# Performance work log

Hardware: AMD Instinct MI355X
Metric: run time of the kernel (lower is better)

The kernel has to match this reference:

```python
import jax, jax.numpy as jnp
import numpy as np

B, T, I, H, O = 64, 2048, 16, 256, 1


def _gru_layer(x, Wih, Whh, bih, bhh):
    # x: [B, T, in]; Wih: [3H, in]; Whh: [3H, H]
    xg = jnp.einsum('bti,gi->btg', x, Wih) + bih  # [B, T, 3H] precomputed input gates

    def step(h, xg_t):
        gh = h @ Whh.T + bhh  # [B, 3H]
        xr, xz, xn = jnp.split(xg_t, 3, axis=-1)
        hr, hz, hn = jnp.split(gh, 3, axis=-1)
        r = jax.nn.sigmoid(xr + hr)
        z = jax.nn.sigmoid(xz + hz)
        n = jnp.tanh(xn + r * hn)
        h_new = (1.0 - z) * n + z * h
        return h_new, h_new

    h0 = jnp.zeros((x.shape[0], Whh.shape[1]), dtype=x.dtype)
    _, hs = jax.lax.scan(step, h0, jnp.swapaxes(xg, 0, 1))  # [T, B, H]
    return jnp.swapaxes(hs, 0, 1)  # [B, T, H]


def setup_inputs() -> dict:
    key = jax.random.key(0)
    ks = jax.random.split(key, 8)

    def xavier(k, shape):
        fan_out, fan_in = shape
        lim = float(np.sqrt(6.0 / (fan_in + fan_out)))
        return jax.random.uniform(k, shape, jnp.float32, -lim, lim)

    return {
        'x': jax.random.normal(ks[0], (B, T, I), jnp.float32),
        'Wih0': xavier(ks[1], (3 * H, I)),
        'Whh0': xavier(ks[2], (3 * H, H)),
        'bih0': jnp.zeros((3 * H,), jnp.float32),
        'bhh0': jnp.zeros((3 * H,), jnp.float32),
        'Wih1': xavier(ks[3], (3 * H, H)),
        'Whh1': xavier(ks[4], (3 * H, H)),
        'bih1': jnp.zeros((3 * H,), jnp.float32),
        'bhh1': jnp.zeros((3 * H,), jnp.float32),
        'W1': xavier(ks[5], (H, H)),
        'b1': jnp.zeros((H,), jnp.float32),
        'W2': xavier(ks[6], (O, H)),
        'b2': jnp.zeros((O,), jnp.float32),
    }


def reference(x, Wih0, Whh0, bih0, bhh0, Wih1, Whh1, bih1, bhh1, W1, b1, W2, b2):
    h1 = _gru_layer(x, Wih0, Whh0, bih0, bhh0)    # layer 0: [B, T, H]
    h2 = _gru_layer(h1, Wih1, Whh1, bih1, bhh1)   # layer 1: [B, T, H]
    r = jax.nn.relu(jnp.einsum('bth,oh->bto', h2, W1) + b1)
    out = jnp.einsum('bth,oh->bto', r, W2) + b2
    return jax.nn.relu(out)  # final relu in forward, [B, T, O]
```

## Files before the change

### kernel.cpp

```cpp
#include <hip/hip_runtime.h>
#include <hip/hip_fp16.h>
#include <stdint.h>

#define B_ 64
#define T_ 2048
#define I_ 16
#define H_ 256
#define G_ 768

#define REC_SMEM 156736

typedef _Float16 f16;
typedef _Float16 half2_t __attribute__((ext_vector_type(2)));
typedef uint32_t u32x4 __attribute__((ext_vector_type(4)));
typedef uint32_t u32x2 __attribute__((ext_vector_type(2)));

__device__ __forceinline__ float fast_rcp(float x) {
#if __has_builtin(__builtin_amdgcn_rcpf)
    return __builtin_amdgcn_rcpf(x);
#else
    return 1.0f / x;
#endif
}
__device__ __forceinline__ float sigmoid_f(float x) {
    return fast_rcp(1.0f + __expf(-x));
}
__device__ __forceinline__ float tanh_f(float x) {
    float e = __expf(2.0f * x);
    return 1.0f - 2.0f * fast_rcp(e + 1.0f);
}

__device__ __forceinline__ float fdot2(uint32_t a, uint32_t b, float c) {
#if __has_builtin(__builtin_amdgcn_fdot2)
    return __builtin_amdgcn_fdot2(__builtin_bit_cast(half2_t, a),
                                  __builtin_bit_cast(half2_t, b), c, false);
#else
    half2_t ha = __builtin_bit_cast(half2_t, a), hb = __builtin_bit_cast(half2_t, b);
    return c + (float)ha.x * (float)hb.x + (float)ha.y * (float)hb.y;
#endif
}
__device__ __forceinline__ float dot_u4(u32x4 w, u32x4 h, float acc) {
    acc = fdot2(w.x, h.x, acc);
    acc = fdot2(w.y, h.y, acc);
    acc = fdot2(w.z, h.z, acc);
    acc = fdot2(w.w, h.w, acc);
    return acc;
}

__global__ __launch_bounds__(256) void cvt_weights(const float* __restrict__ whh0,
                                                   const float* __restrict__ whh1,
                                                   const float* __restrict__ wih1,
                                                   const float* __restrict__ w1,
                                                   uint32_t* __restrict__ out) {
    int idx = blockIdx.x * 256 + threadIdx.x;
    if (idx >= 294912) return;
    if (idx < 163840) {
        const float* w = (idx < 81920) ? whh0 : whh1;
        int l = (idx < 81920) ? idx : idx - 81920;
        if (l < 65536) {
            int u4 = l >> 2, d = l & 3;
            int P = u4 >> 9, t = u4 & 511;
            int j = t >> 1, hf = t & 1;
            int row = (P < 16) ? (256 + j) : (512 + j);
            int u = (P < 16) ? P : P - 16;
            const float* s = w + (size_t)row * 256 + hf * 128 + u * 8 + d * 2;
            half2_t h;
            h.x = (f16)s[0];
            h.y = (f16)s[1];
            out[idx] = __builtin_bit_cast(uint32_t, h);
        } else {
            int l2 = l - 65536;
            int P8 = l2 >> 10, wd = l2 & 1023;
            int t = wd >> 1, piece = wd & 1;
            int j = t >> 1, hf = t & 1;
            const float* s = w + (size_t)j * 256 + hf * 128 + P8 * 8 + piece * 4;
            uint32_t dw = 0;
            #pragma unroll
            for (int k = 0; k < 4; ++k) {
                f16 hh = (f16)s[k];
                uint16_t hb = __builtin_bit_cast(uint16_t, hh);
                uint16_t r8 = (uint16_t)((hb + 0x7F + ((hb >> 8) & 1)) >> 8);
                dw |= (uint32_t)(r8 & 0xFF) << (8 * k);
            }
            out[idx] = dw;
        }
    } else if (idx < 262144) {
        int local = idx - 163840;
        int u4 = local >> 2, d = local & 3;
        int k8 = u4 / 768, g = u4 - k8 * 768;
        const float* s = wih1 + (size_t)g * 256 + k8 * 8 + d * 2;
        half2_t h; h.x = (f16)s[0]; h.y = (f16)s[1];
        out[idx] = __builtin_bit_cast(uint32_t, h);
    } else {
        int local = idx - 262144;
        int u4 = local >> 2, d = local & 3;
        int k8 = u4 >> 8, g = u4 & 255;
        const float* s = w1 + (size_t)g * 256 + k8 * 8 + d * 2;
        half2_t h; h.x = (f16)s[0]; h.y = (f16)s[1];
        out[idx] = __builtin_bit_cast(uint32_t, h);
    }
}


__device__ __forceinline__ void xg0_body(const float* __restrict__ x,
        const float* __restrict__ wih0, const float* __restrict__ bih0,
        float* __restrict__ xg, int t0, int C, int blk, char* smem) {
    float (*xs)[16] = (float(*)[16])smem;
    int tid = threadIdx.x;
    int m0 = blk * 64;
    if (tid < 256) {
        int r = tid >> 2, c4 = (tid & 3) * 4;
        int m = m0 + r;
        int b = m / C, tl = m - b * C;
        float4 v = *(const float4*)(x + (size_t)(b * T_ + t0 + tl) * I_ + c4);
        *(float4*)&xs[r][c4] = v;
    }
    __syncthreads();
    for (int g = tid; g < G_; g += 512) {
        const float4* wr = (const float4*)(wih0 + (size_t)g * I_);
        float4 w0 = wr[0], w1 = wr[1], w2 = wr[2], w3 = wr[3];
        float bias = bih0[g];
        float* outp = xg + (size_t)m0 * G_ + g;
        for (int m = 0; m < 64; ++m) {
            const float4* xr4 = (const float4*)xs[m];
            float4 a0 = xr4[0], a1 = xr4[1], a2 = xr4[2], a3 = xr4[3];
            float acc = bias;
            acc += a0.x*w0.x + a0.y*w0.y + a0.z*w0.z + a0.w*w0.w;
            acc += a1.x*w1.x + a1.y*w1.y + a1.z*w1.z + a1.w*w1.w;
            acc += a2.x*w2.x + a2.y*w2.y + a2.z*w2.z + a2.w*w2.w;
            acc += a3.x*w3.x + a3.y*w3.y + a3.z*w3.z + a3.w*w3.w;
            outp[(size_t)m * G_] = acc;
        }
    }
}

__device__ __forceinline__ void xg1_body(const f16* __restrict__ h1,
        const uint32_t* __restrict__ wih1T, const float* __restrict__ bih1,
        float* __restrict__ xg, int C, int lgC, int blk, char* smem) {
    u32x4 (*hs)[32] = (u32x4(*)[32])smem;
    int tid = threadIdx.x;
    int m0 = (blk & (C - 1)) * 64;
    int gbase = (blk >> lgC) * 256;
    const u32x4* hsrc = (const u32x4*)h1 + (size_t)m0 * 32;
    #pragma unroll
    for (int it = 0; it < 4; ++it) {
        int o = tid + it * 512;
        hs[o >> 5][o & 31] = hsrc[o];
    }
    __syncthreads();
    int gg = tid & 31, mg = tid >> 5;
    const u32x4* wt = (const u32x4*)wih1T;
    float acc[8][4];
    #pragma unroll
    for (int i = 0; i < 8; ++i)
        #pragma unroll
        for (int r = 0; r < 4; ++r) acc[i][r] = 0.0f;
    for (int k8 = 0; k8 < 32; ++k8) {
        u32x4 w[8], h[4];
        #pragma unroll
        for (int i = 0; i < 8; ++i) w[i] = wt[(size_t)k8 * 768 + gbase + gg + 32 * i];
        #pragma unroll
        for (int r = 0; r < 4; ++r) h[r] = hs[mg * 4 + r][k8];
        #pragma unroll
        for (int i = 0; i < 8; ++i)
            #pragma unroll
            for (int r = 0; r < 4; ++r)
                acc[i][r] = dot_u4(w[i], h[r], acc[i][r]);
    }
    #pragma unroll
    for (int i = 0; i < 8; ++i) {
        int g = gbase + gg + 32 * i;
        float bias = bih1[g];
        #pragma unroll
        for (int r = 0; r < 4; ++r)
            xg[(size_t)(m0 + mg * 4 + r) * G_ + g] = acc[i][r] + bias;
    }
}

__device__ __forceinline__ void reg_body(const f16* __restrict__ h2,
        const uint32_t* __restrict__ w1T, const float* __restrict__ b1,
        const float* __restrict__ w2, const float* __restrict__ b2,
        float* __restrict__ out, int t0, int C, int lgC, int blk, char* smem) {
    u32x4 (*hs)[32] = (u32x4(*)[32])smem;
    float (*red)[4] = (float(*)[4])(smem + 32768);
    int tid = threadIdx.x;
    int m0 = blk * 64;
    const u32x4* hsrc = (const u32x4*)h2 + (size_t)m0 * 32;
    #pragma unroll
    for (int it = 0; it < 4; ++it) {
        int o = tid + it * 512;
        hs[o >> 5][o & 31] = hsrc[o];
    }
    __syncthreads();
    int gg = tid & 31, mg = tid >> 5;
    const u32x4* wt = (const u32x4*)w1T;
    float acc[8][4];
    #pragma unroll
    for (int i = 0; i < 8; ++i)
        #pragma unroll
        for (int r = 0; r < 4; ++r) acc[i][r] = 0.0f;
    for (int k8 = 0; k8 < 32; ++k8) {
        u32x4 w[8], h[4];
        #pragma unroll
        for (int i = 0; i < 8; ++i) w[i] = wt[(size_t)k8 * 256 + gg + 32 * i];
        #pragma unroll
        for (int r = 0; r < 4; ++r) h[r] = hs[mg * 4 + r][k8];
        #pragma unroll
        for (int i = 0; i < 8; ++i)
            #pragma unroll
            for (int r = 0; r < 4; ++r)
                acc[i][r] = dot_u4(w[i], h[r], acc[i][r]);
    }
    float pv[4] = {0, 0, 0, 0};
    #pragma unroll
    for (int i = 0; i < 8; ++i) {
        int g = gg + 32 * i;
        float bias = b1[g], w2g = w2[g];
        #pragma unroll
        for (int r = 0; r < 4; ++r)
            pv[r] += w2g * fmaxf(acc[i][r] + bias, 0.0f);
    }
    #pragma unroll
    for (int r = 0; r < 4; ++r) {
        pv[r] += __shfl_xor(pv[r], 1, 64);
        pv[r] += __shfl_xor(pv[r], 2, 64);
        pv[r] += __shfl_xor(pv[r], 4, 64);
        pv[r] += __shfl_xor(pv[r], 8, 64);
        pv[r] += __shfl_xor(pv[r], 16, 64);
    }
    if (gg == 0) {
        #pragma unroll
        for (int r = 0; r < 4; ++r) red[mg][r] = pv[r];
    }
    __syncthreads();
    if (tid < 64) {
        int m = m0 + tid;
        float v = fmaxf(red[tid >> 2][tid & 3] + b2[0], 0.0f);
        int b = m >> lgC, tl = m & (C - 1);
        out[(size_t)b * T_ + t0 + tl] = v;
    }
}

__device__ __forceinline__ void rec_body(const uint32_t* __restrict__ whh,
        const float* __restrict__ bhh, const float* __restrict__ xg,
        f16* __restrict__ hout, float* __restrict__ state,
        int b, int C, char* smem) {
    int tid = threadIdx.x;
    int j = tid >> 1, hf = tid & 1;
    const u32x4* wb = (const u32x4*)whh;
    const u32x2* w8 = (const u32x2*)(whh + 65536);
    u32x4* wlds = (u32x4*)smem;
    u32x4 (*hq)[2][17] = (u32x4(*)[2][17])(smem + 155648);

    #pragma unroll
    for (int s = 0; s < 16; ++s)
        wlds[s * 512 + tid] = wb[(16 + s) * 512 + tid];
    #pragma unroll
    for (int s = 0; s < 3; ++s)
        wlds[(16 + s) * 512 + tid] = wb[(12 + s) * 512 + tid];

    u32x4 Z0  = wb[ 0 * 512 + tid], Z1  = wb[ 1 * 512 + tid];
    u32x4 Z2  = wb[ 2 * 512 + tid], Z3  = wb[ 3 * 512 + tid];
    u32x4 Z4  = wb[ 4 * 512 + tid], Z5  = wb[ 5 * 512 + tid];
    u32x4 Z6  = wb[ 6 * 512 + tid], Z7  = wb[ 7 * 512 + tid];
    u32x4 Z8  = wb[ 8 * 512 + tid], Z9  = wb[ 9 * 512 + tid];
    u32x4 Z10 = wb[10 * 512 + tid], Z11 = wb[11 * 512 + tid];

    float h_old = 0.0f, bhr = 0.0f, bhz = 0.0f, bhn = 0.0f;
    if (hf == 0) {
        h_old = state[b * 256 + j];
        bhr = bhh[j]; bhz = bhh[256 + j]; bhn = bhh[512 + j];
        ((f16*)&hq[0][j >> 7][0])[j & 127] = (f16)h_old;
    }
    __syncthreads();

    const float* xgt = xg + (size_t)b * C * G_;
    f16* hob = hout + (size_t)b * C * H_;
    const u32x4* nl = wlds + tid;

    for (int tl = 0; tl < C; ++tl) {
        int p = tl & 1;
        u32x2 F0  = w8[ 0 * 512 + tid], F1  = w8[ 1 * 512 + tid];
        u32x2 F2  = w8[ 2 * 512 + tid], F3  = w8[ 3 * 512 + tid];
        u32x2 F4  = w8[ 4 * 512 + tid], F5  = w8[ 5 * 512 + tid];
        u32x2 F6  = w8[ 6 * 512 + tid], F7  = w8[ 7 * 512 + tid];
        u32x2 F8  = w8[ 8 * 512 + tid], F9  = w8[ 9 * 512 + tid];
        u32x2 F10 = w8[10 * 512 + tid], F11 = w8[11 * 512 + tid];
        u32x2 F12 = w8[12 * 512 + tid], F13 = w8[13 * 512 + tid];
        u32x2 F14 = w8[14 * 512 + tid], F15 = w8[15 * 512 + tid];
        u32x4 SZ = wb[15 * 512 + tid];
        float xr = 0, xz = 0, xn = 0;
        if (hf == 0) { xr = xgt[j]; xz = xgt[256 + j]; xn = xgt[512 + j]; }

        const u32x4* hp = &hq[p][hf][0];
        float aR = 0.0f, aZ = 0.0f, aN = 0.0f;

#define PU(u, ZS) { u32x4 hv = hp[u]; \
        aN = dot_u4(nl[(u) * 512], hv, aN); \
        aZ = dot_u4(ZS, hv, aZ); \
        u32x4 wr; \
        wr.x = __byte_perm(F##u.x, 0u, 0x1404); \
        wr.y = __byte_perm(F##u.x, 0u, 0x3424); \
        wr.z = __byte_perm(F##u.y, 0u, 0x1404); \
        wr.w = __byte_perm(F##u.y, 0u, 0x3424); \
        aR = dot_u4(wr, hv, aR); }

        PU(0,  Z0)  PU(1,  Z1)  PU(2,  Z2)  PU(3,  Z3)
        PU(4,  Z4)  PU(5,  Z5)  PU(6,  Z6)  PU(7,  Z7)
        PU(8,  Z8)  PU(9,  Z9)  PU(10, Z10) PU(11, Z11)
        PU(12, nl[16 * 512]) PU(13, nl[17 * 512]) PU(14, nl[18 * 512])
        PU(15, SZ)
#undef PU

        aR += __shfl_xor(aR, 1, 64);
        aZ += __shfl_xor(aZ, 1, 64);
        aN += __shfl_xor(aN, 1, 64);

        if (hf == 0) {
            float r = sigmoid_f(xr + aR + bhr);
            float z = sigmoid_f(xz + aZ + bhz);
            float n = tanh_f(xn + r * (aN + bhn));
            h_old = z * (h_old - n) + n;
            f16 hh = (f16)h_old;
            hob[(size_t)tl * H_ + j] = hh;
            ((f16*)&hq[p ^ 1][j >> 7][0])[j & 127] = hh;
        }
        __syncthreads();
        xgt += G_;
    }
    if (hf == 0) state[b * 256 + j] = h_old;
}

__global__ __launch_bounds__(512)
__attribute__((amdgpu_waves_per_eu(2, 2)))
void fused_step(int i, int nC, int C, int lgC,
        const float* __restrict__ x,
        const float* __restrict__ wih0, const float* __restrict__ bih0,
        const uint32_t* __restrict__ whh0, const float* __restrict__ bhh0,
        const uint32_t* __restrict__ whh1, const float* __restrict__ bhh1,
        const uint32_t* __restrict__ wih1T, const float* __restrict__ bih1,
        const uint32_t* __restrict__ w1T, const float* __restrict__ b1,
        const float* __restrict__ w2, const float* __restrict__ b2,
        float* __restrict__ xg0a, float* __restrict__ xg0b,
        float* __restrict__ xg1a, float* __restrict__ xg1b,
        f16* __restrict__ h1a, f16* __restrict__ h1b,
        f16* __restrict__ h2a, f16* __restrict__ h2b,
        float* __restrict__ st0, float* __restrict__ st1,
        float* __restrict__ out) {
    extern __shared__ __align__(16) char smem[];
    int blk = blockIdx.x;
    if (blk < 64) {
        if (i >= nC) return;
        rec_body(whh0, bhh0, (i & 1) ? xg0b : xg0a,
                 (i & 1) ? h1b : h1a, st0, blk, C, smem);
    } else if (blk < 128) {
        int c = i - 2;
        if (c < 0 || c >= nC) return;
        rec_body(whh1, bhh1, (c & 1) ? xg1b : xg1a,
                 (c & 1) ? h2b : h2a, st1, blk - 64, C, smem);
    } else if (blk < 128 + C) {
        int c = i + 1;
        if (c >= nC) return;
        xg0_body(x, wih0, bih0, (c & 1) ? xg0b : xg0a, c * C, C, blk - 128, smem);
    } else if (blk < 128 + 4 * C) {
        int c = i - 1;
        if (c < 0 || c >= nC) return;
        xg1_body((c & 1) ? h1b : h1a, wih1T, bih1,
                 (c & 1) ? xg1b : xg1a, C, lgC, blk - 128 - C, smem);
    } else {
        int c = i - 3;
        if (c < 0 || c >= nC) return;
        reg_body((c & 1) ? h2b : h2a, w1T, b1, w2, b2, out, c * C, C, lgC,
                 blk - 128 - 4 * C, smem);
    }
}

__global__ __launch_bounds__(512) void xg0_stand(const float* __restrict__ x,
        const float* __restrict__ wih0, const float* __restrict__ bih0,
        float* __restrict__ xg, int t0, int C) {
    __shared__ __align__(16) char smem[4096];
    xg0_body(x, wih0, bih0, xg, t0, C, blockIdx.x, smem);
}

extern "C" void kernel_launch(void* const* d_in, const int* in_sizes, int n_in,
                              void* d_out, int out_size, void* d_ws, size_t ws_size,
                              hipStream_t stream) {
    const float* x    = (const float*)d_in[0];
    const float* Wih0 = (const float*)d_in[1];
    const float* Whh0 = (const float*)d_in[2];
    const float* bih0 = (const float*)d_in[3];
    const float* bhh0 = (const float*)d_in[4];
    const float* Wih1 = (const float*)d_in[5];
    const float* Whh1 = (const float*)d_in[6];
    const float* bih1 = (const float*)d_in[7];
    const float* bhh1 = (const float*)d_in[8];
    const float* W1   = (const float*)d_in[9];
    const float* b1   = (const float*)d_in[10];
    const float* W2   = (const float*)d_in[11];
    const float* b2   = (const float*)d_in[12];
    float* out = (float*)d_out;

    hipFuncSetAttribute(reinterpret_cast<const void*>(fused_step),
                        hipFuncAttributeMaxDynamicSharedMemorySize, REC_SMEM);

    char* ws = (char*)d_ws;
    uint32_t* wcvt = (uint32_t*)ws;
    const uint32_t* whh0c = wcvt;
    const uint32_t* whh1c = wcvt + 81920;
    const uint32_t* wih1T = wcvt + 163840;
    const uint32_t* w1T   = wcvt + 262144;
    float* state0 = (float*)(ws + 1179648);
    float* state1 = (float*)(ws + 1179648 + 65536);
    size_t fixed = 1179648 + 2 * 65536;

    int C = 128;
    while (C > 32 && fixed + (size_t)C * 917504 > ws_size) C >>= 1;
    int lgC = 0; while ((1 << lgC) < C) lgC++;
    int nC = T_ / C;

    char* p = ws + fixed;
    float* xg0_buf[2]; float* xg1_buf[2];
    f16* h1_buf[2]; f16* h2_buf[2];
    xg0_buf[0] = (float*)p;  p += (size_t)C * 196608;
    xg0_buf[1] = (float*)p;  p += (size_t)C * 196608;
    xg1_buf[0] = (float*)p;  p += (size_t)C * 196608;
    xg1_buf[1] = (float*)p;  p += (size_t)C * 196608;
    h1_buf[0] = (f16*)p;     p += (size_t)C * 32768;
    h1_buf[1] = (f16*)p;     p += (size_t)C * 32768;
    h2_buf[0] = (f16*)p;     p += (size_t)C * 32768;
    h2_buf[1] = (f16*)p;

    cvt_weights<<<1152, 256, 0, stream>>>(Whh0, Whh1, Wih1, W1, wcvt);
    hipMemsetAsync(state0, 0, 2 * 65536, stream);
    xg0_stand<<<C, 512, 0, stream>>>(x, Wih0, bih0, xg0_buf[0], 0, C);

    for (int i = 0; i <= nC + 2; ++i) {
        fused_step<<<128 + 5 * C, 512, REC_SMEM, stream>>>(i, nC, C, lgC,
            x, Wih0, bih0, whh0c, bhh0, whh1c, bhh1, wih1T, bih1, w1T, b1, W2, b2,
            xg0_buf[0], xg0_buf[1], xg1_buf[0], xg1_buf[1],
            h1_buf[0], h1_buf[1], h2_buf[0], h2_buf[1],
            state0, state1, out);
    }
}
```

Baseline: 2.788 ms.

## Process two batch rows per recurrent block to reuse Whh weights

Each recurrent block now advances two batch sequences at once, so every weight fragment loaded from registers, LDS or global memory feeds two dot products. The recurrent grid halves from 128 to 64 blocks and the weight placement is rebalanced: fewer Z registers, a smaller LDS weight region, and more rows streamed from global each step to make room for the doubled accumulators and h buffers. Amortising weight traffic over two sequences trades per-step latency and register pressure for fewer blocks and less total weight bandwidth, while leaving more CUs free for the other pipeline stages.

New measurement: 8.773 ms. +214.6%, slower.

```diff
diff --git a/kernel.cpp b/kernel.cpp
--- a/kernel.cpp
+++ b/kernel.cpp
@@ -8,7 +8,7 @@
 #define H_ 256
 #define G_ 768
 
-#define REC_SMEM 156736
+#define REC_SMEM 156160
 
 typedef _Float16 f16;
 typedef _Float16 half2_t __attribute__((ext_vector_type(2)));
@@ -244,42 +244,46 @@
 __device__ __forceinline__ void rec_body(const uint32_t* __restrict__ whh,
         const float* __restrict__ bhh, const float* __restrict__ xg,
         f16* __restrict__ hout, float* __restrict__ state,
-        int b, int C, char* smem) {
+        int b0, int C, char* smem) {
     int tid = threadIdx.x;
     int j = tid >> 1, hf = tid & 1;
     const u32x4* wb = (const u32x4*)whh;
     const u32x2* w8 = (const u32x2*)(whh + 65536);
     u32x4* wlds = (u32x4*)smem;
-    u32x4 (*hq)[2][17] = (u32x4(*)[2][17])(smem + 155648);
+    u32x4 (*hq)[2][2][17] = (u32x4(*)[2][2][17])(smem + 147456);
 
     #pragma unroll
     for (int s = 0; s < 16; ++s)
         wlds[s * 512 + tid] = wb[(16 + s) * 512 + tid];
-    #pragma unroll
-    for (int s = 0; s < 3; ++s)
-        wlds[(16 + s) * 512 + tid] = wb[(12 + s) * 512 + tid];
-
-    u32x4 Z0  = wb[ 0 * 512 + tid], Z1  = wb[ 1 * 512 + tid];
-    u32x4 Z2  = wb[ 2 * 512 + tid], Z3  = wb[ 3 * 512 + tid];
-    u32x4 Z4  = wb[ 4 * 512 + tid], Z5  = wb[ 5 * 512 + tid];
-    u32x4 Z6  = wb[ 6 * 512 + tid], Z7  = wb[ 7 * 512 + tid];
-    u32x4 Z8  = wb[ 8 * 512 + tid], Z9  = wb[ 9 * 512 + tid];
-    u32x4 Z10 = wb[10 * 512 + tid], Z11 = wb[11 * 512 + tid];
-
-    float h_old = 0.0f, bhr = 0.0f, bhz = 0.0f, bhn = 0.0f;
+    wlds[16 * 512 + tid] = wb[8 * 512 + tid];
+    wlds[17 * 512 + tid] = wb[9 * 512 + tid];
+
+    u32x4 Z0 = wb[0 * 512 + tid], Z1 = wb[1 * 512 + tid];
+    u32x4 Z2 = wb[2 * 512 + tid], Z3 = wb[3 * 512 + tid];
+    u32x4 Z4 = wb[4 * 512 + tid], Z5 = wb[5 * 512 + tid];
+    u32x4 Z6 = wb[6 * 512 + tid], Z7 = wb[7 * 512 + tid];
+
+    float h0 = 0.0f, h1 = 0.0f, bhr = 0.0f, bhz = 0.0f, bhn = 0.0f;
     if (hf == 0) {
-        h_old = state[b * 256 + j];
+        h0 = state[b0 * 256 + j];
+        h1 = state[(b0 + 1) * 256 + j];
         bhr = bhh[j]; bhz = bhh[256 + j]; bhn = bhh[512 + j];
-        ((f16*)&hq[0][j >> 7][0])[j & 127] = (f16)h_old;
+        ((f16*)&hq[0][0][j >> 7][0])[j & 127] = (f16)h0;
+        ((f16*)&hq[1][0][j >> 7][0])[j & 127] = (f16)h1;
     }
     __syncthreads();
 
-    const float* xgt = xg + (size_t)b * C * G_;
-    f16* hob = hout + (size_t)b * C * H_;
+    const float* xgt0 = xg + (size_t)b0 * C * G_;
+    const float* xgt1 = xgt0 + (size_t)C * G_;
+    f16* hob0 = hout + (size_t)b0 * C * H_;
+    f16* hob1 = hob0 + (size_t)C * H_;
     const u32x4* nl = wlds + tid;
 
     for (int tl = 0; tl < C; ++tl) {
         int p = tl & 1;
+        u32x4 S10 = wb[10 * 512 + tid], S11 = wb[11 * 512 + tid];
+        u32x4 S12 = wb[12 * 512 + tid], S13 = wb[13 * 512 + tid];
+        u32x4 S14 = wb[14 * 512 + tid], S15 = wb[15 * 512 + tid];
         u32x2 F0  = w8[ 0 * 512 + tid], F1  = w8[ 1 * 512 + tid];
         u32x2 F2  = w8[ 2 * 512 + tid], F3  = w8[ 3 * 512 + tid];
         u32x2 F4  = w8[ 4 * 512 + tid], F5  = w8[ 5 * 512 + tid];
@@ -288,47 +292,65 @@
         u32x2 F10 = w8[10 * 512 + tid], F11 = w8[11 * 512 + tid];
         u32x2 F12 = w8[12 * 512 + tid], F13 = w8[13 * 512 + tid];
         u32x2 F14 = w8[14 * 512 + tid], F15 = w8[15 * 512 + tid];
-        u32x4 SZ = wb[15 * 512 + tid];
-        float xr = 0, xz = 0, xn = 0;
-        if (hf == 0) { xr = xgt[j]; xz = xgt[256 + j]; xn = xgt[512 + j]; }
-
-        const u32x4* hp = &hq[p][hf][0];
-        float aR = 0.0f, aZ = 0.0f, aN = 0.0f;
-
-#define PU(u, ZS) { u32x4 hv = hp[u]; \
-        aN = dot_u4(nl[(u) * 512], hv, aN); \
-        aZ = dot_u4(ZS, hv, aZ); \
+        float xr0 = 0, xz0 = 0, xn0 = 0, xr1 = 0, xz1 = 0, xn1 = 0;
+        if (hf == 0) {
+            xr0 = xgt0[j]; xz0 = xgt0[256 + j]; xn0 = xgt0[512 + j];
+            xr1 = xgt1[j]; xz1 = xgt1[256 + j]; xn1 = xgt1[512 + j];
+        }
+
+        const u32x4* hp0 = &hq[0][p][hf][0];
+        const u32x4* hp1 = &hq[1][p][hf][0];
+        float aR0 = 0, aZ0 = 0, aN0 = 0, aR1 = 0, aZ1 = 0, aN1 = 0;
+
+#define NZ(u, ZS) { u32x4 v0 = hp0[u], v1 = hp1[u]; \
+        u32x4 wn = nl[(u) * 512]; \
+        aN0 = dot_u4(wn, v0, aN0); aN1 = dot_u4(wn, v1, aN1); \
+        aZ0 = dot_u4(ZS, v0, aZ0); aZ1 = dot_u4(ZS, v1, aZ1); }
+        NZ(0, Z0)  NZ(1, Z1)  NZ(2, Z2)  NZ(3, Z3)
+        NZ(4, Z4)  NZ(5, Z5)  NZ(6, Z6)  NZ(7, Z7)
+        NZ(8,  nl[16 * 512]) NZ(9,  nl[17 * 512])
+        NZ(10, S10) NZ(11, S11) NZ(12, S12) NZ(13, S13)
+        NZ(14, S14) NZ(15, S15)
+#undef NZ
+
+#define RP(u) { u32x4 v0 = hp0[u], v1 = hp1[u]; \
         u32x4 wr; \
         wr.x = __byte_perm(F##u.x, 0u, 0x1404); \
         wr.y = __byte_perm(F##u.x, 0u, 0x3424); \
         wr.z = __byte_perm(F##u.y, 0u, 0x1404); \
         wr.w = __byte_perm(F##u.y, 0u, 0x3424); \
-        aR = dot_u4(wr, hv, aR); }
-
-        PU(0,  Z0)  PU(1,  Z1)  PU(2,  Z2)  PU(3,  Z3)
-        PU(4,  Z4)  PU(5,  Z5)  PU(6,  Z6)  PU(7,  Z7)
-        PU(8,  Z8)  PU(9,  Z9)  PU(10, Z10) PU(11, Z11)
-        PU(12, nl[16 * 512]) PU(13, nl[17 * 512]) PU(14, nl[18 * 512])
-        PU(15, SZ)
-#undef PU
-
-        aR += __shfl_xor(aR, 1, 64);
-        aZ += __shfl_xor(aZ, 1, 64);
-        aN += __shfl_xor(aN, 1, 64);
+        aR0 = dot_u4(wr, v0, aR0); aR1 = dot_u4(wr, v1, aR1); }
+        RP(0)  RP(1)  RP(2)  RP(3)  RP(4)  RP(5)  RP(6)  RP(7)
+        RP(8)  RP(9)  RP(10) RP(11) RP(12) RP(13) RP(14) RP(15)
+#undef RP
+
+        aR0 += __shfl_xor(aR0, 1, 64); aZ0 += __shfl_xor(aZ0, 1, 64);
+        aN0 += __shfl_xor(aN0, 1, 64);
+        aR1 += __shfl_xor(aR1, 1, 64); aZ1 += __shfl_xor(aZ1, 1, 64);
+        aN1 += __shfl_xor(aN1, 1, 64);
 
         if (hf == 0) {
-            float r = sigmoid_f(xr + aR + bhr);
-            float z = sigmoid_f(xz + aZ + bhz);
-            float n = tanh_f(xn + r * (aN + bhn));
-            h_old = z * (h_old - n) + n;
-            f16 hh = (f16)h_old;
-            hob[(size_t)tl * H_ + j] = hh;
-            ((f16*)&hq[p ^ 1][j >> 7][0])[j & 127] = hh;
+            float r0 = sigmoid_f(xr0 + aR0 + bhr);
+            float z0 = sigmoid_f(xz0 + aZ0 + bhz);
+            float n0 = tanh_f(xn0 + r0 * (aN0 + bhn));
+            h0 = z0 * (h0 - n0) + n0;
+            float r1 = sigmoid_f(xr1 + aR1 + bhr);
+            float z1 = sigmoid_f(xz1 + aZ1 + bhz);
+            float n1 = tanh_f(xn1 + r1 * (aN1 + bhn));
+            h1 = z1 * (h1 - n1) + n1;
+            f16 ha = (f16)h0, hb = (f16)h1;
+            hob0[(size_t)tl * H_ + j] = ha;
+            hob1[(size_t)tl * H_ + j] = hb;
+            ((f16*)&hq[0][p ^ 1][j >> 7][0])[j & 127] = ha;
+            ((f16*)&hq[1][p ^ 1][j >> 7][0])[j & 127] = hb;
         }
         __syncthreads();
-        xgt += G_;
-    }
-    if (hf == 0) state[b * 256 + j] = h_old;
+        xgt0 += G_; xgt1 += G_;
+    }
+    if (hf == 0) {
+        state[b0 * 256 + j] = h0;
+        state[(b0 + 1) * 256 + j] = h1;
+    }
 }
 
 __global__ __launch_bounds__(512)
@@ -349,29 +371,29 @@
         float* __restrict__ out) {
     extern __shared__ __align__(16) char smem[];
     int blk = blockIdx.x;
-    if (blk < 64) {
+    if (blk < 32) {
         if (i >= nC) return;
         rec_body(whh0, bhh0, (i & 1) ? xg0b : xg0a,
-                 (i & 1) ? h1b : h1a, st0, blk, C, smem);
-    } else if (blk < 128) {
+                 (i & 1) ? h1b : h1a, st0, blk * 2, C, smem);
+    } else if (blk < 64) {
         int c = i - 2;
         if (c < 0 || c >= nC) return;
         rec_body(whh1, bhh1, (c & 1) ? xg1b : xg1a,
-                 (c & 1) ? h2b : h2a, st1, blk - 64, C, smem);
-    } else if (blk < 128 + C) {
+                 (c & 1) ? h2b : h2a, st1, (blk - 32) * 2, C, smem);
+    } else if (blk < 64 + C) {
         int c = i + 1;
         if (c >= nC) return;
-        xg0_body(x, wih0, bih0, (c & 1) ? xg0b : xg0a, c * C, C, blk - 128, smem);
-    } else if (blk < 128 + 4 * C) {
+        xg0_body(x, wih0, bih0, (c & 1) ? xg0b : xg0a, c * C, C, blk - 64, smem);
+    } else if (blk < 64 + 4 * C) {
         int c = i - 1;
         if (c < 0 || c >= nC) return;
         xg1_body((c & 1) ? h1b : h1a, wih1T, bih1,
-                 (c & 1) ? xg1b : xg1a, C, lgC, blk - 128 - C, smem);
+                 (c & 1) ? xg1b : xg1a, C, lgC, blk - 64 - C, smem);
     } else {
         int c = i - 3;
         if (c < 0 || c >= nC) return;
         reg_body((c & 1) ? h2b : h2a, w1T, b1, w2, b2, out, c * C, C, lgC,
-                 blk - 128 - 4 * C, smem);
+                 blk - 64 - 4 * C, smem);
     }
 }
 
@@ -435,7 +457,7 @@
     xg0_stand<<<C, 512, 0, stream>>>(x, Wih0, bih0, xg0_buf[0], 0, C);
 
     for (int i = 0; i <= nC + 2; ++i) {
-        fused_step<<<128 + 5 * C, 512, REC_SMEM, stream>>>(i, nC, C, lgC,
+        fused_step<<<64 + 5 * C, 512, REC_SMEM, stream>>>(i, nC, C, lgC,
             x, Wih0, bih0, whh0c, bhh0, whh1c, bhh1, wih1T, bih1, w1T, b1, W2, b2,
             xg0_buf[0], xg0_buf[1], xg1_buf[0], xg1_buf[1],
             h1_buf[0], h1_buf[1], h2_buf[0], h2_buf[1],
```
